# Kernel optimization log

Measured on AMD Instinct MI355X. Metric: run time of the kernel, lower is better.

## Reference

```python
import jax, jax.numpy as jnp
import numpy as np

B, S, D, E, H, K = 2, 2048, 1024, 8, 4096, 2  # batch, seq, n_embed, num_experts, 4*n_embed, top_k


def setup_inputs() -> dict:
    key = jax.random.key(0)
    ks = jax.random.split(key, 10)
    w = lambda k, shape: (jax.random.normal(k, shape, jnp.float32) * 0.02)
    return {
        "x": jax.random.normal(ks[0], (B, S, D), jnp.float32),
        "noise": jax.random.normal(ks[1], (B, S, E), jnp.float32),  # replaces torch.randn_like
        "Wr": w(ks[2], (D, E)),  # topkroute_linear
        "br": jnp.zeros((E,), jnp.float32),
        "Wn": w(ks[3], (D, E)),  # noise_linear
        "bn": jnp.zeros((E,), jnp.float32),
        "W1": w(ks[4], (E, D, H)),  # per-expert first Linear
        "b1": jnp.zeros((E, H), jnp.float32),
        "W2": w(ks[5], (E, H, D)),  # per-expert second Linear
        "b2": jnp.zeros((E, D), jnp.float32),
    }


def reference(x, noise, Wr, br, Wn, bn, W1, b1, W2, b2):
    # --- NoisyTopkRouter ---
    logits = jnp.einsum('bsd,de->bse', x, Wr) + br
    noise_logits = jnp.einsum('bsd,de->bse', x, Wn) + bn
    noisy_logits = logits + noise * jax.nn.softplus(noise_logits)
    _, topi = jax.lax.top_k(noisy_logits, K)                      # [B,S,K]
    sel = (topi[..., :, None] == jnp.arange(E)).any(axis=-2)      # [B,S,E] bool
    gates = jax.nn.softmax(jnp.where(sel, noisy_logits, -jnp.inf), axis=-1)  # sparse softmax
    softmax_gating = jax.nn.softmax(logits, axis=-1)

    # --- expert dispatch: gate is exactly 0 for non-selected experts, so the
    # masked gather/scatter loop equals a gate-weighted sum over all experts ---
    h = jax.nn.relu(jnp.einsum('bsd,edh->ebsh', x, W1) + b1[:, None, None, :])  # [E,B,S,H]
    y = jnp.einsum('ebsh,ehd->ebsd', h, W2) + b2[:, None, None, :]              # [E,B,S,D]
    final = jnp.einsum('bse,ebsd->bsd', gates, y)
    return final, softmax_gating
```

## Files before the change

### kernel.cpp

```cpp
#include <hip/hip_runtime.h>
#include <stdint.h>

#define T_TOK 4096
#define Dm    1024
#define Em    8
#define Hm    4096
#define NSLOT (2 * T_TOK)
#define KSPLIT 2

typedef __bf16 bf16x8 __attribute__((ext_vector_type(8)));
typedef float  f32x4  __attribute__((ext_vector_type(4)));

__device__ __forceinline__ unsigned short f2bf(float f) {
  union { float f; unsigned int u; } c; c.f = f;
  unsigned int u = c.u;
  unsigned int r = u + 0x7fffu + ((u >> 16) & 1u);
  return (unsigned short)(r >> 16);
}

__device__ __forceinline__ void async16(const void* g, void* l) {
  __builtin_amdgcn_global_load_lds(
      (const __attribute__((address_space(1))) void*)g,
      (__attribute__((address_space(3))) void*)l, 16, 0, 0);
}

__global__ __launch_bounds__(256) void transpose_cvt_kernel(
    const float* __restrict__ src, unsigned short* __restrict__ dst, int R, int C) {
  __shared__ float tile[64][65];
  const int e = blockIdx.z;
  const float* s = src + (size_t)e * R * C;
  unsigned short* d = dst + (size_t)e * R * C;
  const int c0 = blockIdx.x * 64, r0 = blockIdx.y * 64;
  const int tid = threadIdx.x;

  const int lr = tid >> 4, lc4 = (tid & 15) * 4;
#pragma unroll
  for (int p = 0; p < 4; ++p) {
    const int r = lr + p * 16;
    float4 v = *(const float4*)(s + (size_t)(r0 + r) * C + c0 + lc4);
    tile[r][lc4 + 0] = v.x; tile[r][lc4 + 1] = v.y;
    tile[r][lc4 + 2] = v.z; tile[r][lc4 + 3] = v.w;
  }
  __syncthreads();

  const int oc = tid >> 3;
  const int rb = (tid & 7) * 4;
#pragma unroll
  for (int p = 0; p < 4; ++p) {
    const int c = oc + (p & 1) * 32;
    const int rr = rb + (p >> 1) * 32;
    ushort4 o;
    o.x = f2bf(tile[rr + 0][c]);
    o.y = f2bf(tile[rr + 1][c]);
    o.z = f2bf(tile[rr + 2][c]);
    o.w = f2bf(tile[rr + 3][c]);
    *(ushort4*)(d + (size_t)(c0 + c) * R + r0 + rr) = o;
  }
}

__global__ void cvt_x_kernel(const float* __restrict__ x, unsigned short* __restrict__ xbf) {
  const int i = blockIdx.x * 256 + threadIdx.x;
  float4 v = ((const float4*)x)[i];
  ushort4 o;
  o.x = f2bf(v.x); o.y = f2bf(v.y); o.z = f2bf(v.z); o.w = f2bf(v.w);
  ((ushort4*)xbf)[i] = o;
}

__global__ __launch_bounds__(256) void router_kernel(
    const float* __restrict__ x, const float* __restrict__ noise,
    const float* __restrict__ Wr, const float* __restrict__ br,
    const float* __restrict__ Wn, const float* __restrict__ bn,
    float* __restrict__ out_gating, int* __restrict__ lists,
    int* __restrict__ counts, int* __restrict__ expt,
    int* __restrict__ pos, float* __restrict__ gsel) {
  const int wave = threadIdx.x >> 6, lane = threadIdx.x & 63;
  const int t = blockIdx.x * 4 + wave;
  const float* xt = x + (size_t)t * Dm;
  float accR[Em] = {}, accN[Em] = {};
  for (int d = lane; d < Dm; d += 64) {
    const float xv = xt[d];
    const float* wr = Wr + d * Em;
    const float* wn = Wn + d * Em;
#pragma unroll
    for (int e = 0; e < Em; e++) { accR[e] += xv * wr[e]; accN[e] += xv * wn[e]; }
  }
#pragma unroll
  for (int e = 0; e < Em; e++)
    for (int off = 32; off > 0; off >>= 1) {
      accR[e] += __shfl_down(accR[e], off, 64);
      accN[e] += __shfl_down(accN[e], off, 64);
    }
  if (lane == 0) {
    float lg[Em], ny[Em];
#pragma unroll
    for (int e = 0; e < Em; e++) {
      lg[e] = accR[e] + br[e];
      float nl = accN[e] + bn[e];
      float sp = fmaxf(nl, 0.f) + log1pf(expf(-fabsf(nl)));
      ny[e] = lg[e] + noise[(size_t)t * Em + e] * sp;
    }
    int i0 = 0;
#pragma unroll
    for (int e = 1; e < Em; e++) if (ny[e] > ny[i0]) i0 = e;
    int i1 = (i0 == 0) ? 1 : 0;
#pragma unroll
    for (int e = 0; e < Em; e++) if (e != i0 && ny[e] > ny[i1]) i1 = e;
    const float e1 = expf(ny[i1] - ny[i0]);
    const float g0 = 1.f / (1.f + e1), g1 = e1 / (1.f + e1);
    float m = lg[0];
#pragma unroll
    for (int e = 1; e < Em; e++) m = fmaxf(m, lg[e]);
    float s = 0.f;
#pragma unroll
    for (int e = 0; e < Em; e++) s += expf(lg[e] - m);
#pragma unroll
    for (int e = 0; e < Em; e++) out_gating[(size_t)t * Em + e] = expf(lg[e] - m) / s;
    int p0 = atomicAdd(&counts[i0], 1); lists[i0 * T_TOK + p0] = t;
    int p1 = atomicAdd(&counts[i1], 1); lists[i1 * T_TOK + p1] = t;
    expt[2 * t] = i0; expt[2 * t + 1] = i1;
    pos[2 * t] = p0;  pos[2 * t + 1] = p1;
    gsel[2 * t] = g0; gsel[2 * t + 1] = g1;
  }
}

__global__ __launch_bounds__(256) void gemm1_kernel(
    const unsigned short* __restrict__ xbf, const unsigned short* __restrict__ w1bf,
    const float* __restrict__ b1, const int* __restrict__ counts,
    const int* __restrict__ lists, unsigned short* __restrict__ hbuf) {
  const int e = blockIdx.x;
  const int cnt = counts[e];
  const int m0 = blockIdx.y * 128;
  if (m0 >= cnt) return;
  const int n0 = blockIdx.z * 128;
  int base = 0;
  for (int i = 0; i < e; i++) base += counts[i];

  __shared__ __align__(16) unsigned short As[3][128 * 32];
  __shared__ __align__(16) unsigned short Bs[3][128 * 32];
  __shared__ int tok[128];

  const int tid = threadIdx.x;
  if (tid < 128) {
    int m = m0 + tid;
    tok[tid] = (m < cnt) ? lists[e * T_TOK + m] : 0;
  }
  __syncthreads();

  const int part = tid & 3;
  const int r0 = tid >> 2;
  const int r1 = r0 + 64;
  const size_t gA0 = (size_t)tok[r0] * Dm + part * 8;
  const size_t gA1 = (size_t)tok[r1] * Dm + part * 8;
  const size_t gB0 = ((size_t)e * Hm + n0 + r0) * Dm + part * 8;
  const size_t gB1 = ((size_t)e * Hm + n0 + r1) * Dm + part * 8;

  const int lane = tid & 63, wv = tid >> 6;
  const int quad = lane >> 4, l15 = lane & 15;
  const int wm = (wv >> 1) * 64, wn = (wv & 1) * 64;
  const int lds_off = wv * 512;

  f32x4 acc[4][4] = {};

  async16(xbf + gA0,       As[0] + lds_off);
  async16(xbf + gA1,       As[0] + 2048 + lds_off);
  async16(w1bf + gB0,      Bs[0] + lds_off);
  async16(w1bf + gB1,      Bs[0] + 2048 + lds_off);
  async16(xbf + gA0 + 32,  As[1] + lds_off);
  async16(xbf + gA1 + 32,  As[1] + 2048 + lds_off);
  async16(w1bf + gB0 + 32, Bs[1] + lds_off);
  async16(w1bf + gB1 + 32, Bs[1] + 2048 + lds_off);

  const int NI = Dm / 32;
  int cur = 0;
  for (int it = 0; it < NI; ++it) {
    if (it < NI - 1) {
      asm volatile("s_waitcnt vmcnt(4)" ::: "memory");
    } else {
      asm volatile("s_waitcnt vmcnt(0)" ::: "memory");
    }
    __builtin_amdgcn_s_barrier();
    __builtin_amdgcn_sched_barrier(0);
    if (it + 2 < NI) {
      const int k0 = (it + 2) * 32;
      int nb = cur + 2; if (nb >= 3) nb -= 3;
      async16(xbf + gA0 + k0, As[nb] + lds_off);
      async16(xbf + gA1 + k0, As[nb] + 2048 + lds_off);
      async16(w1bf + gB0 + k0, Bs[nb] + lds_off);
      async16(w1bf + gB1 + k0, Bs[nb] + 2048 + lds_off);
    }
    bf16x8 af[4], bfv[4];
#pragma unroll
    for (int i = 0; i < 4; i++)
      af[i] = *(const bf16x8*)(As[cur] + (wm + i * 16 + l15) * 32 + quad * 8);
#pragma unroll
    for (int j = 0; j < 4; j++)
      bfv[j] = *(const bf16x8*)(Bs[cur] + (wn + j * 16 + l15) * 32 + quad * 8);
#pragma unroll
    for (int i = 0; i < 4; i++)
#pragma unroll
      for (int j = 0; j < 4; j++)
        acc[i][j] = __builtin_amdgcn_mfma_f32_16x16x32_bf16(af[i], bfv[j], acc[i][j], 0, 0, 0);
    cur = (cur == 2) ? 0 : cur + 1;
  }

#pragma unroll
  for (int i = 0; i < 4; i++)
#pragma unroll
    for (int r = 0; r < 4; r++) {
      const int ml = wm + i * 16 + quad * 4 + r;
      const int m = m0 + ml;
      if (m < cnt) {
#pragma unroll
        for (int j = 0; j < 4; j++) {
          const int n = n0 + wn + j * 16 + l15;
          float v = acc[i][j][r] + b1[(size_t)e * Hm + n];
          v = fmaxf(v, 0.f);
          hbuf[(size_t)(base + m) * Hm + n] = f2bf(v);
        }
      }
    }
}

__global__ __launch_bounds__(256) void gemm2_kernel(
    const unsigned short* __restrict__ hbuf, const unsigned short* __restrict__ w2bf,
    const int* __restrict__ counts, float* __restrict__ ybuf) {
  const int e = blockIdx.x;
  const int ks = blockIdx.z & 1;
  const int cnt = counts[e];
  const int m0 = blockIdx.y * 128;
  if (m0 >= cnt) return;
  const int n0 = (blockIdx.z >> 1) * 128;
  int base = 0;
  for (int i = 0; i < e; i++) base += counts[i];
  const int kbase = ks * (Hm / KSPLIT);

  __shared__ __align__(16) unsigned short As[3][128 * 32];
  __shared__ __align__(16) unsigned short Bs[3][128 * 32];

  const int tid = threadIdx.x;
  const int part = tid & 3;
  const int r0 = tid >> 2;
  const int r1 = r0 + 64;
  const int rowA0 = min(base + m0 + r0, NSLOT - 1);
  const int rowA1 = min(base + m0 + r1, NSLOT - 1);
  const size_t gA0 = (size_t)rowA0 * Hm + kbase + part * 8;
  const size_t gA1 = (size_t)rowA1 * Hm + kbase + part * 8;
  const size_t gB0 = ((size_t)e * Dm + n0 + r0) * Hm + kbase + part * 8;
  const size_t gB1 = ((size_t)e * Dm + n0 + r1) * Hm + kbase + part * 8;

  const int lane = tid & 63, wv = tid >> 6;
  const int quad = lane >> 4, l15 = lane & 15;
  const int wm = (wv >> 1) * 64, wn = (wv & 1) * 64;
  const int lds_off = wv * 512;

  f32x4 acc[4][4] = {};

  async16(hbuf + gA0,       As[0] + lds_off);
  async16(hbuf + gA1,       As[0] + 2048 + lds_off);
  async16(w2bf + gB0,       Bs[0] + lds_off);
  async16(w2bf + gB1,       Bs[0] + 2048 + lds_off);
  async16(hbuf + gA0 + 32,  As[1] + lds_off);
  async16(hbuf + gA1 + 32,  As[1] + 2048 + lds_off);
  async16(w2bf + gB0 + 32,  Bs[1] + lds_off);
  async16(w2bf + gB1 + 32,  Bs[1] + 2048 + lds_off);

  const int NI = Hm / KSPLIT / 32;
  int cur = 0;
  for (int it = 0; it < NI; ++it) {
    if (it < NI - 1) {
      asm volatile("s_waitcnt vmcnt(4)" ::: "memory");
    } else {
      asm volatile("s_waitcnt vmcnt(0)" ::: "memory");
    }
    __builtin_amdgcn_s_barrier();
    __builtin_amdgcn_sched_barrier(0);
    if (it + 2 < NI) {
      const int k0 = (it + 2) * 32;
      int nb = cur + 2; if (nb >= 3) nb -= 3;
      async16(hbuf + gA0 + k0, As[nb] + lds_off);
      async16(hbuf + gA1 + k0, As[nb] + 2048 + lds_off);
      async16(w2bf + gB0 + k0, Bs[nb] + lds_off);
      async16(w2bf + gB1 + k0, Bs[nb] + 2048 + lds_off);
    }
    bf16x8 af[4], bfv[4];
#pragma unroll
    for (int i = 0; i < 4; i++)
      af[i] = *(const bf16x8*)(As[cur] + (wm + i * 16 + l15) * 32 + quad * 8);
#pragma unroll
    for (int j = 0; j < 4; j++)
      bfv[j] = *(const bf16x8*)(Bs[cur] + (wn + j * 16 + l15) * 32 + quad * 8);
#pragma unroll
    for (int i = 0; i < 4; i++)
#pragma unroll
      for (int j = 0; j < 4; j++)
        acc[i][j] = __builtin_amdgcn_mfma_f32_16x16x32_bf16(af[i], bfv[j], acc[i][j], 0, 0, 0);
    cur = (cur == 2) ? 0 : cur + 1;
  }

  float* yb = ybuf + (size_t)ks * NSLOT * Dm;
#pragma unroll
  for (int i = 0; i < 4; i++)
#pragma unroll
    for (int r = 0; r < 4; r++) {
      const int ml = wm + i * 16 + quad * 4 + r;
      const int m = m0 + ml;
      if (m < cnt) {
#pragma unroll
        for (int j = 0; j < 4; j++) {
          const int n = n0 + wn + j * 16 + l15;
          yb[(size_t)(base + m) * Dm + n] = acc[i][j][r];
        }
      }
    }
}

__global__ __launch_bounds__(256) void combine_kernel(
    const float* __restrict__ ybuf, const float* __restrict__ b2,
    const int* __restrict__ counts, const int* __restrict__ expt,
    const int* __restrict__ pos, const float* __restrict__ gsel,
    float* __restrict__ out) {
  const int t = blockIdx.x;
  const int e0 = expt[2 * t], e1 = expt[2 * t + 1];
  const float g0 = gsel[2 * t], g1 = gsel[2 * t + 1];
  int b0 = 0, b1 = 0;
  for (int i = 0; i < e0; i++) b0 += counts[i];
  for (int i = 0; i < e1; i++) b1 += counts[i];
  const size_t s0 = (size_t)(b0 + pos[2 * t]) * Dm;
  const size_t s1 = (size_t)(b1 + pos[2 * t + 1]) * Dm;
  const size_t half = (size_t)NSLOT * Dm;
  const int c = threadIdx.x * 4;
  float4 y0a = *(const float4*)(ybuf + s0 + c);
  float4 y0b = *(const float4*)(ybuf + half + s0 + c);
  float4 y1a = *(const float4*)(ybuf + s1 + c);
  float4 y1b = *(const float4*)(ybuf + half + s1 + c);
  float4 z0 = *(const float4*)(b2 + (size_t)e0 * Dm + c);
  float4 z1 = *(const float4*)(b2 + (size_t)e1 * Dm + c);
  float4 o;
  o.x = g0 * (y0a.x + y0b.x + z0.x) + g1 * (y1a.x + y1b.x + z1.x);
  o.y = g0 * (y0a.y + y0b.y + z0.y) + g1 * (y1a.y + y1b.y + z1.y);
  o.z = g0 * (y0a.z + y0b.z + z0.z) + g1 * (y1a.z + y1b.z + z1.z);
  o.w = g0 * (y0a.w + y0b.w + z0.w) + g1 * (y1a.w + y1b.w + z1.w);
  *(float4*)(out + (size_t)t * Dm + c) = o;
}

extern "C" void kernel_launch(void* const* d_in, const int* in_sizes, int n_in,
                              void* d_out, int out_size, void* d_ws, size_t ws_size,
                              hipStream_t stream) {
  const float* x     = (const float*)d_in[0];
  const float* noise = (const float*)d_in[1];
  const float* Wr    = (const float*)d_in[2];
  const float* br    = (const float*)d_in[3];
  const float* Wn    = (const float*)d_in[4];
  const float* bn    = (const float*)d_in[5];
  const float* W1    = (const float*)d_in[6];
  const float* b1    = (const float*)d_in[7];
  const float* W2    = (const float*)d_in[8];
  const float* b2    = (const float*)d_in[9];

  float* out        = (float*)d_out;
  float* out_gating = out + (size_t)T_TOK * Dm;

  char* ws = (char*)d_ws;
  unsigned short* w1bf = (unsigned short*)(ws);
  unsigned short* w2bf = (unsigned short*)(ws + 67108864);
  unsigned short* xbf  = (unsigned short*)(ws + 134217728);
  unsigned short* hbuf = (unsigned short*)(ws + 142606336);
  float* ybuf          = (float*)(ws);
  int*   lists         = (int*)(ws + 209715200);
  int*   expt          = (int*)(ws + 209846272);
  int*   pos           = (int*)(ws + 209879040);
  float* gsel          = (float*)(ws + 209911808);
  int*   counts        = (int*)(ws + 209944576);

  hipMemsetAsync(counts, 0, Em * sizeof(int), stream);

  transpose_cvt_kernel<<<dim3(Hm / 64, Dm / 64, Em), 256, 0, stream>>>(W1, w1bf, Dm, Hm);
  transpose_cvt_kernel<<<dim3(Dm / 64, Hm / 64, Em), 256, 0, stream>>>(W2, w2bf, Hm, Dm);
  cvt_x_kernel<<<(T_TOK * Dm / 4) / 256, 256, 0, stream>>>(x, xbf);

  router_kernel<<<T_TOK / 4, 256, 0, stream>>>(x, noise, Wr, br, Wn, bn,
                                               out_gating, lists, counts, expt, pos, gsel);

  gemm1_kernel<<<dim3(Em, 16, Hm / 128), 256, 0, stream>>>(xbf, w1bf, b1, counts, lists, hbuf);
  gemm2_kernel<<<dim3(Em, 16, (Dm / 128) * KSPLIT), 256, 0, stream>>>(hbuf, w2bf, counts, ybuf);
  combine_kernel<<<T_TOK, 256, 0, stream>>>(ybuf, b2, counts, expt, pos, gsel, out);
}
```

Baseline: 724.4 us.

## Fuse combine into gemm2 via atomic scatter and fold x cast into router

After: 753.9 us. 1.04x slower.

```diff
diff --git a/kernel.cpp b/kernel.cpp
--- a/kernel.cpp
+++ b/kernel.cpp
@@ -10,6 +10,7 @@
 
 typedef __bf16 bf16x8 __attribute__((ext_vector_type(8)));
 typedef float  f32x4  __attribute__((ext_vector_type(4)));
+typedef unsigned short us8v __attribute__((ext_vector_type(8)));
 
 __device__ __forceinline__ unsigned short f2bf(float f) {
   union { float f; unsigned int u; } c; c.f = f;
@@ -26,44 +27,32 @@
 
 __global__ __launch_bounds__(256) void transpose_cvt_kernel(
     const float* __restrict__ src, unsigned short* __restrict__ dst, int R, int C) {
-  __shared__ float tile[64][65];
+  __shared__ float tile[128][33];
   const int e = blockIdx.z;
   const float* s = src + (size_t)e * R * C;
   unsigned short* d = dst + (size_t)e * R * C;
-  const int c0 = blockIdx.x * 64, r0 = blockIdx.y * 64;
+  const int c0 = blockIdx.x * 32, r0 = blockIdx.y * 128;
   const int tid = threadIdx.x;
 
-  const int lr = tid >> 4, lc4 = (tid & 15) * 4;
+  const int lrow = tid >> 3, lc = (tid & 7) * 4;
 #pragma unroll
   for (int p = 0; p < 4; ++p) {
-    const int r = lr + p * 16;
-    float4 v = *(const float4*)(s + (size_t)(r0 + r) * C + c0 + lc4);
-    tile[r][lc4 + 0] = v.x; tile[r][lc4 + 1] = v.y;
-    tile[r][lc4 + 2] = v.z; tile[r][lc4 + 3] = v.w;
+    const int row = lrow + p * 32;
+    float4 v = *(const float4*)(s + (size_t)(r0 + row) * C + c0 + lc);
+    tile[row][lc + 0] = v.x; tile[row][lc + 1] = v.y;
+    tile[row][lc + 2] = v.z; tile[row][lc + 3] = v.w;
   }
   __syncthreads();
 
-  const int oc = tid >> 3;
-  const int rb = (tid & 7) * 4;
-#pragma unroll
-  for (int p = 0; p < 4; ++p) {
-    const int c = oc + (p & 1) * 32;
-    const int rr = rb + (p >> 1) * 32;
-    ushort4 o;
-    o.x = f2bf(tile[rr + 0][c]);
-    o.y = f2bf(tile[rr + 1][c]);
-    o.z = f2bf(tile[rr + 2][c]);
-    o.w = f2bf(tile[rr + 3][c]);
-    *(ushort4*)(d + (size_t)(c0 + c) * R + r0 + rr) = o;
-  }
-}
-
-__global__ void cvt_x_kernel(const float* __restrict__ x, unsigned short* __restrict__ xbf) {
-  const int i = blockIdx.x * 256 + threadIdx.x;
-  float4 v = ((const float4*)x)[i];
-  ushort4 o;
-  o.x = f2bf(v.x); o.y = f2bf(v.y); o.z = f2bf(v.z); o.w = f2bf(v.w);
-  ((ushort4*)xbf)[i] = o;
+  const int rb = (tid & 15) * 8;
+#pragma unroll
+  for (int p = 0; p < 2; ++p) {
+    const int c = (tid >> 4) + p * 16;
+    us8v o;
+#pragma unroll
+    for (int k = 0; k < 8; ++k) o[k] = f2bf(tile[rb + k][c]);
+    *(us8v*)(d + (size_t)(c0 + c) * R + r0 + rb) = o;
+  }
 }
 
 __global__ __launch_bounds__(256) void router_kernel(
@@ -71,14 +60,15 @@
     const float* __restrict__ Wr, const float* __restrict__ br,
     const float* __restrict__ Wn, const float* __restrict__ bn,
     float* __restrict__ out_gating, int* __restrict__ lists,
-    int* __restrict__ counts, int* __restrict__ expt,
-    int* __restrict__ pos, float* __restrict__ gsel) {
+    int* __restrict__ counts, float* __restrict__ gslot,
+    unsigned short* __restrict__ xbf) {
   const int wave = threadIdx.x >> 6, lane = threadIdx.x & 63;
   const int t = blockIdx.x * 4 + wave;
   const float* xt = x + (size_t)t * Dm;
   float accR[Em] = {}, accN[Em] = {};
   for (int d = lane; d < Dm; d += 64) {
     const float xv = xt[d];
+    xbf[(size_t)t * Dm + d] = f2bf(xv);
     const float* wr = Wr + d * Em;
     const float* wn = Wn + d * Em;
 #pragma unroll
@@ -117,9 +107,8 @@
     for (int e = 0; e < Em; e++) out_gating[(size_t)t * Em + e] = expf(lg[e] - m) / s;
     int p0 = atomicAdd(&counts[i0], 1); lists[i0 * T_TOK + p0] = t;
     int p1 = atomicAdd(&counts[i1], 1); lists[i1 * T_TOK + p1] = t;
-    expt[2 * t] = i0; expt[2 * t + 1] = i1;
-    pos[2 * t] = p0;  pos[2 * t + 1] = p1;
-    gsel[2 * t] = g0; gsel[2 * t + 1] = g1;
+    gslot[i0 * T_TOK + p0] = g0;
+    gslot[i1 * T_TOK + p1] = g1;
   }
 }
 
@@ -223,7 +212,9 @@
 
 __global__ __launch_bounds__(256) void gemm2_kernel(
     const unsigned short* __restrict__ hbuf, const unsigned short* __restrict__ w2bf,
-    const int* __restrict__ counts, float* __restrict__ ybuf) {
+    const int* __restrict__ counts, const int* __restrict__ lists,
+    const float* __restrict__ gslot, const float* __restrict__ b2,
+    float* __restrict__ out) {
   const int e = blockIdx.x;
   const int ks = blockIdx.z & 1;
   const int cnt = counts[e];
@@ -236,8 +227,17 @@
 
   __shared__ __align__(16) unsigned short As[3][128 * 32];
   __shared__ __align__(16) unsigned short Bs[3][128 * 32];
+  __shared__ int tok[128];
+  __shared__ float gt[128];
 
   const int tid = threadIdx.x;
+  if (tid < 128) {
+    int m = m0 + tid;
+    tok[tid] = (m < cnt) ? lists[e * T_TOK + m] : 0;
+    gt[tid]  = (m < cnt) ? gslot[e * T_TOK + m] : 0.f;
+  }
+  __syncthreads();
+
   const int part = tid & 3;
   const int r0 = tid >> 2;
   const int r1 = r0 + 64;
@@ -297,7 +297,6 @@
     cur = (cur == 2) ? 0 : cur + 1;
   }
 
-  float* yb = ybuf + (size_t)ks * NSLOT * Dm;
 #pragma unroll
   for (int i = 0; i < 4; i++)
 #pragma unroll
@@ -305,42 +304,18 @@
       const int ml = wm + i * 16 + quad * 4 + r;
       const int m = m0 + ml;
       if (m < cnt) {
+        const int t = tok[ml];
+        const float g = gt[ml];
+        float* orow = out + (size_t)t * Dm + n0;
 #pragma unroll
         for (int j = 0; j < 4; j++) {
-          const int n = n0 + wn + j * 16 + l15;
-          yb[(size_t)(base + m) * Dm + n] = acc[i][j][r];
+          const int n = wn + j * 16 + l15;
+          float v = acc[i][j][r];
+          if (ks == 0) v += b2[(size_t)e * Dm + n0 + n];
+          atomicAdd(orow + n, g * v);
         }
       }
     }
-}
-
-__global__ __launch_bounds__(256) void combine_kernel(
-    const float* __restrict__ ybuf, const float* __restrict__ b2,
-    const int* __restrict__ counts, const int* __restrict__ expt,
-    const int* __restrict__ pos, const float* __restrict__ gsel,
-    float* __restrict__ out) {
-  const int t = blockIdx.x;
-  const int e0 = expt[2 * t], e1 = expt[2 * t + 1];
-  const float g0 = gsel[2 * t], g1 = gsel[2 * t + 1];
-  int b0 = 0, b1 = 0;
-  for (int i = 0; i < e0; i++) b0 += counts[i];
-  for (int i = 0; i < e1; i++) b1 += counts[i];
-  const size_t s0 = (size_t)(b0 + pos[2 * t]) * Dm;
-  const size_t s1 = (size_t)(b1 + pos[2 * t + 1]) * Dm;
-  const size_t half = (size_t)NSLOT * Dm;
-  const int c = threadIdx.x * 4;
-  float4 y0a = *(const float4*)(ybuf + s0 + c);
-  float4 y0b = *(const float4*)(ybuf + half + s0 + c);
-  float4 y1a = *(const float4*)(ybuf + s1 + c);
-  float4 y1b = *(const float4*)(ybuf + half + s1 + c);
-  float4 z0 = *(const float4*)(b2 + (size_t)e0 * Dm + c);
-  float4 z1 = *(const float4*)(b2 + (size_t)e1 * Dm + c);
-  float4 o;
-  o.x = g0 * (y0a.x + y0b.x + z0.x) + g1 * (y1a.x + y1b.x + z1.x);
-  o.y = g0 * (y0a.y + y0b.y + z0.y) + g1 * (y1a.y + y1b.y + z1.y);
-  o.z = g0 * (y0a.z + y0b.z + z0.z) + g1 * (y1a.z + y1b.z + z1.z);
-  o.w = g0 * (y0a.w + y0b.w + z0.w) + g1 * (y1a.w + y1b.w + z1.w);
-  *(float4*)(out + (size_t)t * Dm + c) = o;
 }
 
 extern "C" void kernel_launch(void* const* d_in, const int* in_sizes, int n_in,
@@ -365,23 +340,20 @@
   unsigned short* w2bf = (unsigned short*)(ws + 67108864);
   unsigned short* xbf  = (unsigned short*)(ws + 134217728);
   unsigned short* hbuf = (unsigned short*)(ws + 142606336);
-  float* ybuf          = (float*)(ws);
   int*   lists         = (int*)(ws + 209715200);
-  int*   expt          = (int*)(ws + 209846272);
-  int*   pos           = (int*)(ws + 209879040);
-  float* gsel          = (float*)(ws + 209911808);
-  int*   counts        = (int*)(ws + 209944576);
+  float* gslot         = (float*)(ws + 209846272);
+  int*   counts        = (int*)(ws + 209977344);
 
   hipMemsetAsync(counts, 0, Em * sizeof(int), stream);
-
-  transpose_cvt_kernel<<<dim3(Hm / 64, Dm / 64, Em), 256, 0, stream>>>(W1, w1bf, Dm, Hm);
-  transpose_cvt_kernel<<<dim3(Dm / 64, Hm / 64, Em), 256, 0, stream>>>(W2, w2bf, Hm, Dm);
-  cvt_x_kernel<<<(T_TOK * Dm / 4) / 256, 256, 0, stream>>>(x, xbf);
+  hipMemsetAsync(out, 0, (size_t)T_TOK * Dm * sizeof(float), stream);
+
+  transpose_cvt_kernel<<<dim3(Hm / 32, Dm / 128, Em), 256, 0, stream>>>(W1, w1bf, Dm, Hm);
+  transpose_cvt_kernel<<<dim3(Dm / 32, Hm / 128, Em), 256, 0, stream>>>(W2, w2bf, Hm, Dm);
 
   router_kernel<<<T_TOK / 4, 256, 0, stream>>>(x, noise, Wr, br, Wn, bn,
-                                               out_gating, lists, counts, expt, pos, gsel);
+                                               out_gating, lists, counts, gslot, xbf);
 
   gemm1_kernel<<<dim3(Em, 16, Hm / 128), 256, 0, stream>>>(xbf, w1bf, b1, counts, lists, hbuf);
-  gemm2_kernel<<<dim3(Em, 16, (Dm / 128) * KSPLIT), 256, 0, stream>>>(hbuf, w2bf, counts, ybuf);
-  combine_kernel<<<T_TOK, 256, 0, stream>>>(ybuf, b2, counts, expt, pos, gsel, out);
-}
+  gemm2_kernel<<<dim3(Em, 16, (Dm / 128) * KSPLIT), 256, 0, stream>>>(hbuf, w2bf, counts, lists,
+                                                                      gslot, b2, out);
+}
```
